# Performance work log

Measured on AMD Instinct MI355X. Metric: run time of the kernel, lower is better.

## Reference

```python
import jax, jax.numpy as jnp
import numpy as np


def setup_inputs() -> dict:
    key = jax.random.key(0)
    k1, k2, k3, k4 = jax.random.split(key, 4)
    B, N, D, K, O = 8, 6144, 16, 3, 64
    inputs = jax.random.normal(k1, (B, N, D), dtype=jnp.float32)
    supports = jax.random.uniform(k2, (K, N, N), dtype=jnp.float32)
    W = jax.random.normal(k3, (O, D * K), dtype=jnp.float32) * 0.05
    b = jax.random.normal(k4, (O,), dtype=jnp.float32) * 0.05
    return {"inputs": inputs, "supports": supports, "W": W, "b": b}


def reference(inputs, supports, W, b):
    # inputs: [B, N, D]; supports: [K, N, N]; W: [O, D*K]; b: [O]
    B, N, D = inputs.shape
    K = supports.shape[0]
    # matrix_normalization: support + I  (identity self-loop add)
    sup = supports + jnp.eye(N, dtype=supports.dtype)  # [K, N, N]
    # per-support dense matmul; layout [B, N, D, K] matches the torch
    # stack/reshape/transpose chain (feature index = d*K + k)
    y = jnp.einsum('knm,bmd->bndk', sup, inputs)  # [B, N, D, K]
    y = y.reshape(B, N, D * K)
    return y @ W.T + b  # [B, N, O]
```

## Files before the change

### kernel.cpp

```cpp
#include <hip/hip_runtime.h>

#define NN 6144
#define BND (NN*16)

typedef short short8 __attribute__((ext_vector_type(8)));
typedef float f32x4 __attribute__((ext_vector_type(4)));

__device__ __forceinline__ short f2bf(float f) {
    unsigned u = __builtin_bit_cast(unsigned, f);
    u = (u + 0x7FFFu + ((u >> 16) & 1u)) >> 16;
    return (short)u;
}
__device__ __forceinline__ float bf2f(unsigned short s) {
    unsigned u = ((unsigned)s) << 16;
    return __builtin_bit_cast(float, u);
}

__global__ void __launch_bounds__(256) prep_kernel(
    const float* __restrict__ xin, unsigned short* __restrict__ Xt)
{
    __shared__ unsigned short ldsT[16 * 64];
    const int b  = blockIdx.y;
    const int m0 = blockIdx.x * 64;
    const int t  = threadIdx.x;
    const int ml = t >> 2, dq = t & 3;
    float4 v = *(const float4*)(xin + (size_t)b * BND + (size_t)(m0 + ml) * 16 + dq * 4);
    ldsT[(dq * 4 + 0) * 64 + ml] = (unsigned short)f2bf(v.x);
    ldsT[(dq * 4 + 1) * 64 + ml] = (unsigned short)f2bf(v.y);
    ldsT[(dq * 4 + 2) * 64 + ml] = (unsigned short)f2bf(v.z);
    ldsT[(dq * 4 + 3) * 64 + ml] = (unsigned short)f2bf(v.w);
    __syncthreads();
    if (t < 128) {
        int d = t >> 3, j = t & 7;
        short8 s = *(const short8*)&ldsT[d * 64 + j * 8];
        *(short8*)(Xt + (size_t)(b * 16 + d) * NN + m0 + j * 8) = s;
    }
}


__device__ __forceinline__ void stage_tile(
    const float* __restrict__ Ab, const unsigned short* __restrict__ Xt,
    float* ldsA, unsigned short* ldsB, int n0, int k0, int tid)
{
#pragma unroll
    for (int i = 0; i < 4; ++i) {
        int p = i * 256 + tid;
        int r = p >> 4, cs = p & 15;
        int cch = cs ^ (r & 7);
        const float* src = Ab + (size_t)(n0 + r) * NN + k0 + cch * 4;
        __builtin_amdgcn_global_load_lds(
            (const __attribute__((address_space(1))) unsigned int*)src,
            (__attribute__((address_space(3))) unsigned int*)((char*)ldsA + p * 16), 16, 0, 0);
    }
#pragma unroll
    for (int i = 0; i < 4; ++i) {
        int p = i * 256 + tid;
        int c = p >> 3, hs = p & 7;
        int h = hs ^ (c & 7);
        const unsigned short* src = Xt + (size_t)c * NN + k0 + h * 8;
        __builtin_amdgcn_global_load_lds(
            (const __attribute__((address_space(1))) unsigned int*)src,
            (__attribute__((address_space(3))) unsigned int*)((char*)ldsB + p * 16), 16, 0, 0);
    }
}

__device__ __forceinline__ void compute_tile(
    const float* ldsA, const unsigned short* ldsB,
    int w, int q, int col, f32x4* acc)
{
    const int r = w * 16 + col;
#pragma unroll
    for (int kc = 0; kc < 2; ++kc) {
        int c0 = kc * 8 + q * 2;
        float4 a0 = *(const float4*)&ldsA[(r * 16 + ((c0    ) ^ (r & 7))) * 4];
        float4 a1 = *(const float4*)&ldsA[(r * 16 + ((c0 + 1) ^ (r & 7))) * 4];
        short8 af;
        af[0] = f2bf(a0.x); af[1] = f2bf(a0.y); af[2] = f2bf(a0.z); af[3] = f2bf(a0.w);
        af[4] = f2bf(a1.x); af[5] = f2bf(a1.y); af[6] = f2bf(a1.z); af[7] = f2bf(a1.w);
#pragma unroll
        for (int cc = 0; cc < 8; ++cc) {
            int c = cc * 16 + col;
            short8 bf = *(const short8*)&ldsB[(c * 8 + ((kc * 4 + q) ^ (c & 7))) * 8];
            acc[cc] = __builtin_amdgcn_mfma_f32_16x16x32_bf16(af, bf, acc[cc], 0, 0, 0);
        }
    }
}

__global__ void __launch_bounds__(256, 2) gemm_kernel(
    const float* __restrict__ sup, const unsigned short* __restrict__ Xt,
    unsigned short* __restrict__ Yp)
{
    __shared__ float ldsram[16384];
    float* A0 = ldsram;
    unsigned short* B0 = (unsigned short*)(ldsram + 4096);
    float* A1 = ldsram + 8192;
    unsigned short* B1 = (unsigned short*)(ldsram + 12288);

    const int tid = threadIdx.x;
    const int w = tid >> 6, L = tid & 63, q = L >> 4, col = L & 15;
    const int n0  = blockIdx.x * 64;
    const int k   = blockIdx.y;
    const int seg = blockIdx.z;
    const float* Ab = sup + (size_t)k * NN * NN;
    const int kbase = seg * 3072;

    f32x4 acc[8];
#pragma unroll
    for (int i = 0; i < 8; ++i) acc[i] = (f32x4)0.0f;

    stage_tile(Ab, Xt, A0, B0, n0, kbase, tid);
    asm volatile("s_waitcnt vmcnt(0)" ::: "memory");
    __builtin_amdgcn_s_barrier();

#pragma unroll 1
    for (int it = 0; it < 48; it += 2) {
        stage_tile(Ab, Xt, A1, B1, n0, kbase + (it + 1) * 64, tid);
        __builtin_amdgcn_sched_barrier(0);
        compute_tile(A0, B0, w, q, col, acc);
        asm volatile("s_waitcnt vmcnt(0)" ::: "memory");
        __builtin_amdgcn_s_barrier();
        if (it + 2 < 48) {
            stage_tile(Ab, Xt, A0, B0, n0, kbase + (it + 2) * 64, tid);
            __builtin_amdgcn_sched_barrier(0);
            compute_tile(A1, B1, w, q, col, acc);
            asm volatile("s_waitcnt vmcnt(0)" ::: "memory");
            __builtin_amdgcn_s_barrier();
        } else {
            compute_tile(A1, B1, w, q, col, acc);
        }
    }

    float* stg = ldsram + w * 2048;
#pragma unroll
    for (int cc = 0; cc < 8; ++cc)
#pragma unroll
        for (int rr = 0; rr < 4; ++rr)
            stg[(q * 4 + rr) * 128 + cc * 16 + col] = acc[cc][rr];

    unsigned short* ypb = Yp + ((size_t)(seg * 3 + k) * NN + n0 + w * 16) * 128;
#pragma unroll
    for (int u = 0; u < 8; ++u) {
        int idx = u * 256 + L * 4;
        float4 v = *(const float4*)&stg[idx];
        unsigned h0 = (unsigned short)f2bf(v.x) | ((unsigned)(unsigned short)f2bf(v.y) << 16);
        unsigned h1 = (unsigned short)f2bf(v.z) | ((unsigned)(unsigned short)f2bf(v.w) << 16);
        uint2 pk; pk.x = h0; pk.y = h1;
        *(uint2*)(ypb + idx) = pk;
    }
}

__global__ void __launch_bounds__(256) out_kernel(
    const unsigned short* __restrict__ Yp, const float* __restrict__ xin,
    const float* __restrict__ W, const float* __restrict__ bias, float* __restrict__ out)
{
    const int o   = threadIdx.x & 63;
    const int wid = blockIdx.x * 4 + (threadIdx.x >> 6);

    float wreg[48];
#pragma unroll
    for (int d = 0; d < 16; ++d)
#pragma unroll
        for (int kk = 0; kk < 3; ++kk)
            wreg[kk * 16 + d] = W[o * 48 + d * 3 + kk];
    float wsum[16];
#pragma unroll
    for (int d = 0; d < 16; ++d) wsum[d] = wreg[d] + wreg[16 + d] + wreg[32 + d];
    const float bv = bias[o];

    for (int ii = 0; ii < 24; ++ii) {
        int p = wid * 24 + ii;
        int b = p / NN;
        int n = p - b * NN;
        float acc = bv;
        const float* xp = xin + (size_t)b * BND + (size_t)n * 16;
#pragma unroll
        for (int d4 = 0; d4 < 4; ++d4) {
            float4 x4 = *(const float4*)(xp + d4 * 4);
            acc += x4.x * wsum[d4 * 4] + x4.y * wsum[d4 * 4 + 1]
                 + x4.z * wsum[d4 * 4 + 2] + x4.w * wsum[d4 * 4 + 3];
        }
#pragma unroll
        for (int s = 0; s < 2; ++s)
#pragma unroll
            for (int kk = 0; kk < 3; ++kk) {
                const unsigned short* yp = Yp + ((size_t)(s * 3 + kk) * NN + n) * 128 + b * 16;
                short8 y0 = *(const short8*)yp;
                short8 y1 = *(const short8*)(yp + 8);
#pragma unroll
                for (int j = 0; j < 8; ++j) {
                    acc += bf2f((unsigned short)y0[j]) * wreg[kk * 16 + j];
                    acc += bf2f((unsigned short)y1[j]) * wreg[kk * 16 + 8 + j];
                }
            }
        out[(size_t)p * 64 + o] = acc;
    }
}

extern "C" void kernel_launch(void* const* d_in, const int* in_sizes, int n_in,
                              void* d_out, int out_size, void* d_ws, size_t ws_size,
                              hipStream_t stream) {
    const float* xin  = (const float*)d_in[0];
    const float* sup  = (const float*)d_in[1];
    const float* W    = (const float*)d_in[2];
    const float* bias = (const float*)d_in[3];
    float* out = (float*)d_out;

    char* ws = (char*)d_ws;
    unsigned short* Xt = (unsigned short*)ws;
    unsigned short* Yp = (unsigned short*)(ws + 1572864);

    prep_kernel<<<dim3(96, 8), 256, 0, stream>>>(xin, Xt);
    gemm_kernel<<<dim3(96, 3, 2), 256, 0, stream>>>(sup, Xt, Yp);
    out_kernel<<<512, 256, 0, stream>>>(Yp, xin, W, bias, out);
}
```

Measured before the change: 743.1 us.

## Switch GEMM to triple-buffered 32-wide K tiles with partial vmcnt waits

The GEMM main loop moves from double-buffered 64-wide K tiles with a full vmcnt(0) wait every step to a three-stage ring of 32-wide K tiles. A partial wait lets the next tile's loads stay in flight while the current tile is computed. The smaller LDS footprint (48KB) and launch_bounds raised to 4 blocks per SM are meant to improve occupancy and hide global memory latency. In exchange there are twice as many barriers per K step, and register pressure under the tighter launch bound may cause spills.

New measurement: 720.5 us. 1.03x faster.

```diff
diff --git a/kernel.cpp b/kernel.cpp
--- a/kernel.cpp
+++ b/kernel.cpp
@@ -38,14 +38,14 @@
 }
 
 
-__device__ __forceinline__ void stage_tile(
+__device__ __forceinline__ void stage_tile32(
     const float* __restrict__ Ab, const unsigned short* __restrict__ Xt,
     float* ldsA, unsigned short* ldsB, int n0, int k0, int tid)
 {
 #pragma unroll
-    for (int i = 0; i < 4; ++i) {
+    for (int i = 0; i < 2; ++i) {
         int p = i * 256 + tid;
-        int r = p >> 4, cs = p & 15;
+        int r = p >> 3, cs = p & 7;
         int cch = cs ^ (r & 7);
         const float* src = Ab + (size_t)(n0 + r) * NN + k0 + cch * 4;
         __builtin_amdgcn_global_load_lds(
@@ -53,10 +53,10 @@
             (__attribute__((address_space(3))) unsigned int*)((char*)ldsA + p * 16), 16, 0, 0);
     }
 #pragma unroll
-    for (int i = 0; i < 4; ++i) {
+    for (int i = 0; i < 2; ++i) {
         int p = i * 256 + tid;
-        int c = p >> 3, hs = p & 7;
-        int h = hs ^ (c & 7);
+        int c = p >> 2, hs = p & 3;
+        int h = hs ^ (c & 3);
         const unsigned short* src = Xt + (size_t)c * NN + k0 + h * 8;
         __builtin_amdgcn_global_load_lds(
             (const __attribute__((address_space(1))) unsigned int*)src,
@@ -64,37 +64,29 @@
     }
 }
 
-__device__ __forceinline__ void compute_tile(
+__device__ __forceinline__ void compute_tile32(
     const float* ldsA, const unsigned short* ldsB,
     int w, int q, int col, f32x4* acc)
 {
     const int r = w * 16 + col;
-#pragma unroll
-    for (int kc = 0; kc < 2; ++kc) {
-        int c0 = kc * 8 + q * 2;
-        float4 a0 = *(const float4*)&ldsA[(r * 16 + ((c0    ) ^ (r & 7))) * 4];
-        float4 a1 = *(const float4*)&ldsA[(r * 16 + ((c0 + 1) ^ (r & 7))) * 4];
-        short8 af;
-        af[0] = f2bf(a0.x); af[1] = f2bf(a0.y); af[2] = f2bf(a0.z); af[3] = f2bf(a0.w);
-        af[4] = f2bf(a1.x); af[5] = f2bf(a1.y); af[6] = f2bf(a1.z); af[7] = f2bf(a1.w);
-#pragma unroll
-        for (int cc = 0; cc < 8; ++cc) {
-            int c = cc * 16 + col;
-            short8 bf = *(const short8*)&ldsB[(c * 8 + ((kc * 4 + q) ^ (c & 7))) * 8];
-            acc[cc] = __builtin_amdgcn_mfma_f32_16x16x32_bf16(af, bf, acc[cc], 0, 0, 0);
-        }
-    }
-}
-
-__global__ void __launch_bounds__(256, 2) gemm_kernel(
+    float4 a0 = *(const float4*)&ldsA[(r * 8 + ((2 * q    ) ^ (r & 7))) * 4];
+    float4 a1 = *(const float4*)&ldsA[(r * 8 + ((2 * q + 1) ^ (r & 7))) * 4];
+    short8 af;
+    af[0] = f2bf(a0.x); af[1] = f2bf(a0.y); af[2] = f2bf(a0.z); af[3] = f2bf(a0.w);
+    af[4] = f2bf(a1.x); af[5] = f2bf(a1.y); af[6] = f2bf(a1.z); af[7] = f2bf(a1.w);
+#pragma unroll
+    for (int cc = 0; cc < 8; ++cc) {
+        int c = cc * 16 + col;
+        short8 bf = *(const short8*)&ldsB[(c * 4 + (q ^ (c & 3))) * 8];
+        acc[cc] = __builtin_amdgcn_mfma_f32_16x16x32_bf16(af, bf, acc[cc], 0, 0, 0);
+    }
+}
+
+__global__ void __launch_bounds__(256, 4) gemm_kernel(
     const float* __restrict__ sup, const unsigned short* __restrict__ Xt,
     unsigned short* __restrict__ Yp)
 {
-    __shared__ float ldsram[16384];
-    float* A0 = ldsram;
-    unsigned short* B0 = (unsigned short*)(ldsram + 4096);
-    float* A1 = ldsram + 8192;
-    unsigned short* B1 = (unsigned short*)(ldsram + 12288);
+    __shared__ float ldsram[12288];
 
     const int tid = threadIdx.x;
     const int w = tid >> 6, L = tid & 63, q = L >> 4, col = L & 15;
@@ -108,26 +100,32 @@
 #pragma unroll
     for (int i = 0; i < 8; ++i) acc[i] = (f32x4)0.0f;
 
-    stage_tile(Ab, Xt, A0, B0, n0, kbase, tid);
+    stage_tile32(Ab, Xt, ldsram,        (unsigned short*)(ldsram + 2048),        n0, kbase,      tid);
+    stage_tile32(Ab, Xt, ldsram + 4096, (unsigned short*)(ldsram + 4096 + 2048), n0, kbase + 32, tid);
+
+    int cur = 0;
+#pragma unroll 1
+    for (int t = 0; t < 95; ++t) {
+        asm volatile("s_waitcnt vmcnt(4)" ::: "memory");
+        __builtin_amdgcn_s_barrier();
+        __builtin_amdgcn_sched_barrier(0);
+        int sd = cur + 2; if (sd >= 3) sd -= 3;
+        if (t + 2 < 96) {
+            float* dA = ldsram + sd * 4096;
+            stage_tile32(Ab, Xt, dA, (unsigned short*)(dA + 2048),
+                         n0, kbase + (t + 2) * 32, tid);
+        }
+        __builtin_amdgcn_sched_barrier(0);
+        const float* cA = ldsram + cur * 4096;
+        compute_tile32(cA, (const unsigned short*)(cA + 2048), w, q, col, acc);
+        cur = (cur == 2) ? 0 : cur + 1;
+    }
     asm volatile("s_waitcnt vmcnt(0)" ::: "memory");
     __builtin_amdgcn_s_barrier();
-
-#pragma unroll 1
-    for (int it = 0; it < 48; it += 2) {
-        stage_tile(Ab, Xt, A1, B1, n0, kbase + (it + 1) * 64, tid);
-        __builtin_amdgcn_sched_barrier(0);
-        compute_tile(A0, B0, w, q, col, acc);
-        asm volatile("s_waitcnt vmcnt(0)" ::: "memory");
-        __builtin_amdgcn_s_barrier();
-        if (it + 2 < 48) {
-            stage_tile(Ab, Xt, A0, B0, n0, kbase + (it + 2) * 64, tid);
-            __builtin_amdgcn_sched_barrier(0);
-            compute_tile(A1, B1, w, q, col, acc);
-            asm volatile("s_waitcnt vmcnt(0)" ::: "memory");
-            __builtin_amdgcn_s_barrier();
-        } else {
-            compute_tile(A1, B1, w, q, col, acc);
-        }
+    __builtin_amdgcn_sched_barrier(0);
+    {
+        const float* cA = ldsram + cur * 4096;
+        compute_tile32(cA, (const unsigned short*)(cA + 2048), w, q, col, acc);
     }
 
     float* stg = ldsram + w * 2048;
```
